# Kernel optimization log

Hardware: AMD Instinct MI355X
Metric: run time of the kernel (lower is better)

The kernel has to match this reference:

```python
import jax, jax.numpy as jnp
import numpy as np

N_USERS = 100000
N_TWEETS = 100000
N_NODES = N_USERS + N_TWEETS
N_EDGES = 600000
D = 128


def lrelu(x):
    return jax.nn.leaky_relu(x, negative_slope=0.01)


def linear(x, W, b):
    # torch nn.Linear convention: W is [out, in]
    return x @ W.T + b


def rgcn_conv(x, edge_index, edge_type, weight, root, bias):
    """PyG RGCNConv with num_relations=2, aggr='mean', root weight + bias."""
    src, dst = edge_index[0], edge_index[1]
    m = x[src]  # [E, D] gathered source features
    out = x @ root + bias
    for r in range(weight.shape[0]):
        mask = (edge_type == r).astype(x.dtype)  # [E]
        s = jax.ops.segment_sum(m * mask[:, None], dst, num_segments=N_NODES)
        cnt = jax.ops.segment_sum(mask, dst, num_segments=N_NODES)
        mean = s / jnp.maximum(cnt, 1.0)[:, None]  # nodes w/o rel-r in-edges -> 0
        out = out + mean @ weight[r]
    return out


def setup_inputs() -> dict:
    key = jax.random.key(0)
    ks = jax.random.split(key, 24)

    def lin(k, out_d, in_d):
        k1, k2 = jax.random.split(k)
        s = 1.0 / np.sqrt(in_d)
        return (jax.random.uniform(k1, (out_d, in_d), jnp.float32, -s, s),
                jax.random.uniform(k2, (out_d,), jnp.float32, -s, s))

    des = jax.random.normal(ks[0], (N_USERS, 100), jnp.float32)
    tweet = jax.random.normal(ks[1], (N_TWEETS, 100), jnp.float32)
    num_prop = jax.random.normal(ks[2], (N_USERS, 6), jnp.float32)
    cat_prop = jax.random.normal(ks[3], (N_USERS, 11), jnp.float32)
    edge_index = jax.random.randint(ks[4], (2, N_EDGES), 0, N_NODES, jnp.int32)
    edge_type = jax.random.randint(ks[5], (N_EDGES,), 0, 2, jnp.int32)

    W_des, b_des = lin(ks[6], D // 2, 100)       # des -> 64
    W_num, b_num = lin(ks[7], D // 4, 6)         # num_prop -> 32
    W_cat, b_cat = lin(ks[8], D // 4, 11)        # cat_prop -> 32
    W_tw, b_tw = lin(ks[9], D, 100)              # tweet -> 128
    W_in, b_in = lin(ks[10], D, D)
    rgcn_w = jax.random.normal(ks[11], (2, D, D), jnp.float32) / np.sqrt(D)
    rgcn_root = jax.random.normal(ks[12], (D, D), jnp.float32) / np.sqrt(D)
    rgcn_bias = jnp.zeros((D,), jnp.float32)
    W_o1, b_o1 = lin(ks[13], D, D)
    W_o2, b_o2 = lin(ks[14], 2, D)

    return dict(des=des, tweet=tweet, num_prop=num_prop, cat_prop=cat_prop,
                edge_index=edge_index, edge_type=edge_type,
                W_des=W_des, b_des=b_des, W_num=W_num, b_num=b_num,
                W_cat=W_cat, b_cat=b_cat, W_tw=W_tw, b_tw=b_tw,
                W_in=W_in, b_in=b_in, rgcn_w=rgcn_w, rgcn_root=rgcn_root,
                rgcn_bias=rgcn_bias, W_o1=W_o1, b_o1=b_o1, W_o2=W_o2, b_o2=b_o2)


def reference(des, tweet, num_prop, cat_prop, edge_index, edge_type,
              W_des, b_des, W_num, b_num, W_cat, b_cat, W_tw, b_tw,
              W_in, b_in, rgcn_w, rgcn_root, rgcn_bias, W_o1, b_o1, W_o2, b_o2):
    d = lrelu(linear(des, W_des, b_des))
    n = lrelu(linear(num_prop, W_num, b_num))
    c = lrelu(linear(cat_prop, W_cat, b_cat))
    x_users = jnp.concatenate([d, n, c], axis=1)       # [N_users, 128]
    t = lrelu(linear(tweet, W_tw, b_tw))               # [N_tweets, 128]
    x = jnp.concatenate([x_users, t], axis=0)          # [N_nodes, 128]
    x = lrelu(linear(x, W_in, b_in))
    x = rgcn_conv(x, edge_index, edge_type, rgcn_w, rgcn_root, rgcn_bias)
    # dropout in eval mode = identity
    x = rgcn_conv(x, edge_index, edge_type, rgcn_w, rgcn_root, rgcn_bias)
    x = lrelu(linear(x, W_o1, b_o1))
    return linear(x, W_o2, b_o2)
```

## Files before the change

### kernel.cpp

```cpp
#include <hip/hip_runtime.h>
#include <hip/hip_bf16.h>

typedef __hip_bfloat16 bf16;

typedef __bf16 bfv8 __attribute__((ext_vector_type(8)));
typedef float f32x4 __attribute__((ext_vector_type(4)));

__device__ __forceinline__ float lrelu(float x) { return x > 0.f ? x : 0.01f * x; }

__device__ __forceinline__ float ldv(float v) { return v; }
__device__ __forceinline__ float ldv(bf16 v) { return __bfloat162float(v); }
__device__ __forceinline__ void stv(float* p, float v) { *p = v; }
__device__ __forceinline__ void stv(bf16* p, float v) { *p = __float2bfloat16(v); }

__device__ __forceinline__ float in_rd(const void* p, size_t i, int isbf) {
  return isbf ? __bfloat162float(((const bf16*)p)[i]) : ((const float*)p)[i];
}
__device__ __forceinline__ int ix_rd(const void* p, size_t i, int is64) {
  return is64 ? (int)((const long long*)p)[i] : ((const int*)p)[i];
}

struct ProbeArgs {
  const void* p[23];
  int s[23];
  int mode[23];
};

__global__ void detect_all(ProbeArgs a, int* __restrict__ flags) {
  __shared__ int sh[256];
  int b = blockIdx.x;
  const unsigned int* w = (const unsigned int*)a.p[b];
  int s = a.s[b], mode = a.mode[b];
  int t = threadIdx.x;
  int c = 0;
  if (t < s) {
    if (mode == 0) {
      unsigned int v = w[t];
      int e = (v >> 7) & 0xFF;
      c = (e >= 100 && e <= 140) ? 1 : 0;
    } else {
      c = (w[2 * t + 1] == 0u) ? 1 : 0;
    }
  }
  sh[t] = c;
  __syncthreads();
  for (int d = 128; d; d >>= 1) {
    if (t < d) sh[t] += sh[t + d];
    __syncthreads();
  }
  if (t == 0) flags[b] = (mode == 0) ? (sh[0] * 10 >= 7 * s) : (sh[0] * 10 >= 9 * s);
}

#define PW_F32 82562
#define BF_BASE 82564
#define PW_W_TOTAL (BF_BASE + 5 * 8192)
#define ENC_BASE PW_W_TOTAL
#define ENC_N 33024
#define PW_TOTAL (ENC_BASE + 16384 + 256)
__global__ void setup_all(const void* Win, const void* bin, const void* rw, const void* root,
                          const void* rb, const void* Wo1, const void* bo1, const void* Wo2,
                          const void* bo2, const void* Wd, const void* bd, const void* Wn,
                          const void* bn, const void* Wc, const void* bc, const void* Wt,
                          const void* bt, const int* __restrict__ fl, int dDes, int dNum,
                          int dCat, int dTw, float* __restrict__ pw, int* __restrict__ cnt4,
                          int NNr) {
  int i = blockIdx.x * 256 + threadIdx.x;
  if (i < PW_W_TOTAL) {
    if (i < 16384) {
      int k = i >> 7, o = i & 127;
      pw[i] = in_rd(Win, (size_t)o * 128 + k, fl[14]);
    } else if (i < 32768) {
      int j = i - 16384;
      int k = j >> 7, o = j & 127;
      pw[i] = in_rd(Wo1, (size_t)o * 128 + k, fl[19]);
    } else if (i < 49152) {
      pw[i] = in_rd(root, i - 32768, fl[17]);
    } else if (i < 81920) {
      pw[i] = in_rd(rw, i - 49152, fl[16]);
    } else if (i < 82048) {
      pw[i] = in_rd(bin, i - 81920, fl[15]);
    } else if (i < 82176) {
      pw[i] = in_rd(rb, i - 82048, fl[18]);
    } else if (i < 82304) {
      pw[i] = in_rd(bo1, i - 82176, fl[20]);
    } else if (i < 82560) {
      pw[i] = in_rd(Wo2, i - 82304, fl[21]);
    } else if (i < PW_F32) {
      pw[i] = in_rd(bo2, i - 82560, fl[22]);
    } else if (i >= BF_BASE) {
      int j = i - BF_BASE;
      bf16* bw = (bf16*)(pw + BF_BASE);
#pragma unroll
      for (int q = 0; q < 2; q++) {
        int u = 2 * j + q;
        int m = u >> 14, r = u & 16383;
        int n = r >> 7, k = r & 127;
        float v;
        if (m == 0) v = in_rd(Win, (size_t)n * 128 + k, fl[14]);
        else if (m == 1) v = in_rd(Wo1, (size_t)n * 128 + k, fl[19]);
        else if (m == 2) v = in_rd(root, (size_t)k * 128 + n, fl[17]);
        else v = in_rd(rw, (size_t)(m - 3) * 16384 + (size_t)k * 128 + n, fl[16]);
        bw[u] = __float2bfloat16(v);
      }
    }
  } else if (i < PW_W_TOTAL + ENC_N) {
    int j = i - PW_W_TOTAL;
    bf16* e = (bf16*)(pw + ENC_BASE);
    float* bU = pw + ENC_BASE + 16384;
    float* bT = bU + 128;
    if (j < 16384) {
      int n = j >> 7, k = j & 127;
      float v = 0.f;
      if (n < 64) {
        if (k < dDes) v = in_rd(Wd, (size_t)n * dDes + k, fl[6]);
      } else if (n < 96) {
        int kk = k - dDes;
        if (kk >= 0 && kk < dNum) v = in_rd(Wn, (size_t)(n - 64) * dNum + kk, fl[8]);
      } else {
        int kk = k - dDes - dNum;
        if (kk >= 0 && kk < dCat) v = in_rd(Wc, (size_t)(n - 96) * dCat + kk, fl[10]);
      }
      e[j] = __float2bfloat16(v);
    } else if (j < 32768) {
      int j2 = j - 16384;
      int n = j2 >> 7, k = j2 & 127;
      float v = (k < dTw) ? in_rd(Wt, (size_t)n * dTw + k, fl[12]) : 0.f;
      e[j] = __float2bfloat16(v);
    } else if (j < 32896) {
      int j2 = j - 32768;
      bU[j2] = (j2 < 64) ? in_rd(bd, j2, fl[7])
                         : (j2 < 96) ? in_rd(bn, j2 - 64, fl[9]) : in_rd(bc, j2 - 96, fl[11]);
    } else {
      bT[j - 32896] = in_rd(bt, j - 32896, fl[13]);
    }
  } else {
    int j = i - PW_W_TOTAL - ENC_N;
    if (j < 4 * NNr) cnt4[j] = 0;
  }
}

__global__ void sig_fill(float* __restrict__ p, int n, float v) {
  int i = blockIdx.x * 256 + threadIdx.x;
  if (i < n) p[i] = v;
}

__global__ void count_edges(const void* __restrict__ ei, const void* __restrict__ et,
                            const int* __restrict__ fl, int* __restrict__ cnt, int NEr,
                            int NNr) {
  int e = blockIdx.x * 256 + threadIdx.x;
  if (e >= NEr) return;
  int d = ix_rd(ei, (size_t)NEr + e, fl[4]);
  int r = ix_rd(et, e, fl[5]) & 1;
  if ((unsigned)d >= (unsigned)NNr) return;
  atomicAdd(&cnt[r * NNr + d], 1);
}

__global__ void scan_blocks(const int* __restrict__ in, int* __restrict__ out,
                            int* __restrict__ bsum, int n) {
  __shared__ int sh[256];
  int t = threadIdx.x;
  int base = blockIdx.x * 1024 + t * 4;
  int a[4];
  int s = 0;
#pragma unroll
  for (int i = 0; i < 4; i++) {
    a[i] = (base + i < n) ? in[base + i] : 0;
    s += a[i];
  }
  sh[t] = s;
  __syncthreads();
  for (int d = 1; d < 256; d <<= 1) {
    int v = (t >= d) ? sh[t - d] : 0;
    __syncthreads();
    sh[t] += v;
    __syncthreads();
  }
  int ex = sh[t] - s;
#pragma unroll
  for (int i = 0; i < 4; i++) {
    if (base + i < n) out[base + i] = ex;
    ex += a[i];
  }
  if (t == 255 && bsum) bsum[blockIdx.x] = sh[255];
}

__global__ void scan_add_inv(int* __restrict__ off, const int* __restrict__ bsumsc,
                             const int* __restrict__ cnt, float* __restrict__ inv, int n) {
  int i = blockIdx.x * 256 + threadIdx.x;
  if (i >= n) return;
  off[i] += bsumsc[i >> 10];
  inv[i] = 1.f / fmaxf((float)cnt[i], 1.f);
}

__global__ void fill_elist(const void* __restrict__ ei, const void* __restrict__ et,
                           const int* __restrict__ fl, const int* __restrict__ off,
                           int* __restrict__ fill, int* __restrict__ elist, int NEr, int NNr) {
  int e = blockIdx.x * 256 + threadIdx.x;
  if (e >= NEr) return;
  int s = ix_rd(ei, e, fl[4]);
  int d = ix_rd(ei, (size_t)NEr + e, fl[4]);
  int r = ix_rd(et, e, fl[5]) & 1;
  if ((unsigned)d >= (unsigned)NNr || (unsigned)s >= (unsigned)NNr) return;
  int idx = r * NNr + d;
  int slot = off[idx] + atomicAdd(&fill[idx], 1);
  elist[slot] = s | ((d & 127) << 24);
}

__global__ __launch_bounds__(256) void enc_gemm(const void* __restrict__ A,
                                                const void* __restrict__ W,
                                                const void* __restrict__ B,
                                                const int* __restrict__ fl, int fa, int fw,
                                                int fb, bf16* __restrict__ x, int M, int K,
                                                int N, int row0, int col0) {
  __shared__ float Wb[128 * 102];
  __shared__ float bb[128];
  int t = threadIdx.x;
  int stride = (K & 1) ? K : K + 1;
  int fA = fl[fa];
  {
    int fW = fl[fw], fB = fl[fb];
    for (int idx = t; idx < N * K; idx += 256) {
      int j = idx / K, k = idx - j * K;
      Wb[j * stride + k] = in_rd(W, (size_t)j * K + k, fW);
    }
    if (t < N) bb[t] = in_rd(B, t, fB);
  }
  __syncthreads();
  int j = t % N;
  int r = t / N;
  int R = 256 / N;
  int iEnd = blockIdx.x * 64 + 64;
  if (iEnd > M) iEnd = M;
  const float* wrow = &Wb[j * stride];
  if (!fA) {
    const float* Af = (const float*)A;
    for (int i = blockIdx.x * 64 + r; i < iEnd; i += R) {
      const float* a = Af + (size_t)i * K;
      float acc = bb[j];
      for (int k = 0; k < K; k++) acc += a[k] * wrow[k];
      stv(&x[(size_t)(row0 + i) * 128 + col0 + j], lrelu(acc));
    }
  } else {
    const bf16* Ab = (const bf16*)A;
    for (int i = blockIdx.x * 64 + r; i < iEnd; i += R) {
      const bf16* a = Ab + (size_t)i * K;
      float acc = bb[j];
      for (int k = 0; k < K; k++) acc += __bfloat162float(a[k]) * wrow[k];
      stv(&x[(size_t)(row0 + i) * 128 + col0 + j], lrelu(acc));
    }
  }
}


__global__ __launch_bounds__(256) void enc_mfma(
    const void* __restrict__ A0, const void* __restrict__ A1, const void* __restrict__ A2,
    const int* __restrict__ fl, int fi0, int fi1, int fi2, int K0, int K1, int K2,
    const bf16* __restrict__ WbE, const float* __restrict__ biasE,
    const bf16* __restrict__ WbL, const float* __restrict__ bL, bf16* __restrict__ x,
    int M, int row0) {
  __shared__ __align__(16) bf16 Xs[16384];
  int t = threadIdx.x;
  int i0 = blockIdx.x * 128;

  {
    uint4 z = {0u, 0u, 0u, 0u};
#pragma unroll
    for (int i = 0; i < 8; i++) *(uint4*)((char*)Xs + i * 4096 + t * 16) = z;
  }
  __syncthreads();

  const void* As[3] = {A0, A1, A2};
  int Ks_[3] = {K0, K1, K2};
  int fis[3] = {fi0, fi1, fi2};
  int cb = 0;
  for (int s = 0; s < 3; s++) {
    int Ks = Ks_[s];
    if (Ks <= 0) continue;
    int isbf = fl[fis[s]];
    int total = 128 * Ks;
    long gml = (long)(M - i0) * Ks;
    int gmax = gml > total ? total : (gml < 0 ? 0 : (int)gml);
    int nu = (total + 3) >> 2;
    if (!isbf) {
      const float* Af = (const float*)As[s] + (size_t)i0 * Ks;
      for (int u = t; u < nu; u += 256) {
        int f0 = u * 4;
        float vv[4];
        if (f0 + 4 <= gmax) {
          float4 x4 = *(const float4*)(Af + f0);
          vv[0] = x4.x; vv[1] = x4.y; vv[2] = x4.z; vv[3] = x4.w;
        } else {
          vv[0] = (f0 < gmax) ? Af[f0] : 0.f;
          vv[1] = (f0 + 1 < gmax) ? Af[f0 + 1] : 0.f;
          vv[2] = (f0 + 2 < gmax) ? Af[f0 + 2] : 0.f;
          vv[3] = (f0 + 3 < gmax) ? Af[f0 + 3] : 0.f;
        }
#pragma unroll
        for (int q = 0; q < 4; q++) {
          int f = f0 + q;
          if (f < total) {
            int row = f / Ks, k = f - row * Ks;
            int byte = row * 256 + (cb + k) * 2;
            *(bf16*)((char*)Xs + (byte ^ ((row & 7) << 4))) = __float2bfloat16(vv[q]);
          }
        }
      }
    } else {
      const unsigned short* Ab = (const unsigned short*)As[s] + (size_t)i0 * Ks;
      for (int u = t; u < nu; u += 256) {
        int f0 = u * 4;
        unsigned short vv[4];
        if (f0 + 4 <= gmax) {
          ushort4 x4 = *(const ushort4*)(Ab + f0);
          vv[0] = x4.x; vv[1] = x4.y; vv[2] = x4.z; vv[3] = x4.w;
        } else {
          vv[0] = (f0 < gmax) ? Ab[f0] : 0;
          vv[1] = (f0 + 1 < gmax) ? Ab[f0 + 1] : 0;
          vv[2] = (f0 + 2 < gmax) ? Ab[f0 + 2] : 0;
          vv[3] = (f0 + 3 < gmax) ? Ab[f0 + 3] : 0;
        }
#pragma unroll
        for (int q = 0; q < 4; q++) {
          int f = f0 + q;
          if (f < total) {
            int row = f / Ks, k = f - row * Ks;
            int byte = row * 256 + (cb + k) * 2;
            *(unsigned short*)((char*)Xs + (byte ^ ((row & 7) << 4))) = vv[q];
          }
        }
      }
    }
    cb += Ks;
  }
  __syncthreads();

  int wv = t >> 6, l = t & 63;
  int lr = l & 15, lg = l >> 4;
  int rbase = (wv >> 1) * 64, cbase = (wv & 1) * 64;
  int ko = lg * 8;
  f32x4 acc[4][4] = {};
#pragma unroll
  for (int ks = 0; ks < 4; ks++) {
    bfv8 bk[4];
#pragma unroll
    for (int cg = 0; cg < 4; cg++)
      bk[cg] = *(const bfv8*)&WbE[(size_t)(cbase + cg * 16 + lr) * 128 + ks * 32 + ko];
    bfv8 af[4];
#pragma unroll
    for (int rg = 0; rg < 4; rg++) {
      int mrow = rbase + rg * 16 + lr;
      int byte = mrow * 256 + (ks * 32 + ko) * 2;
      af[rg] = *(const bfv8*)((const char*)Xs + (byte ^ ((mrow & 7) << 4)));
    }
#pragma unroll
    for (int rg = 0; rg < 4; rg++)
#pragma unroll
      for (int cg = 0; cg < 4; cg++)
        acc[rg][cg] =
            __builtin_amdgcn_mfma_f32_16x16x32_bf16(af[rg], bk[cg], acc[rg][cg], 0, 0, 0);
  }
  __syncthreads();

#pragma unroll
  for (int cg = 0; cg < 4; cg++) {
    int col = cbase + cg * 16 + lr;
    float bv = biasE[col];
#pragma unroll
    for (int rg = 0; rg < 4; rg++) {
      int r0 = rbase + rg * 16 + lg * 4;
#pragma unroll
      for (int j = 0; j < 4; j++) {
        int row = r0 + j;
        int byte = row * 256 + col * 2;
        *(bf16*)((char*)Xs + (byte ^ ((row & 7) << 4))) =
            __float2bfloat16(lrelu(acc[rg][cg][j] + bv));
      }
    }
  }
  __syncthreads();

  f32x4 acc2[4][4] = {};
#pragma unroll
  for (int ks = 0; ks < 4; ks++) {
    bfv8 bk[4];
#pragma unroll
    for (int cg = 0; cg < 4; cg++)
      bk[cg] = *(const bfv8*)&WbL[(size_t)(cbase + cg * 16 + lr) * 128 + ks * 32 + ko];
    bfv8 af[4];
#pragma unroll
    for (int rg = 0; rg < 4; rg++) {
      int mrow = rbase + rg * 16 + lr;
      int byte = mrow * 256 + (ks * 32 + ko) * 2;
      af[rg] = *(const bfv8*)((const char*)Xs + (byte ^ ((mrow & 7) << 4)));
    }
#pragma unroll
    for (int rg = 0; rg < 4; rg++)
#pragma unroll
      for (int cg = 0; cg < 4; cg++)
        acc2[rg][cg] =
            __builtin_amdgcn_mfma_f32_16x16x32_bf16(af[rg], bk[cg], acc2[rg][cg], 0, 0, 0);
  }

#pragma unroll
  for (int cg = 0; cg < 4; cg++) {
    int col = cbase + cg * 16 + lr;
    float bv = bL[col];
#pragma unroll
    for (int rg = 0; rg < 4; rg++) {
      int r0 = i0 + rbase + rg * 16 + lg * 4;
#pragma unroll
      for (int j = 0; j < 4; j++) {
        int row = r0 + j;
        if (row < M)
          x[(size_t)(row0 + row) * 128 + col] = __float2bfloat16(lrelu(acc2[rg][cg][j] + bv));
      }
    }
  }
}

__global__ __launch_bounds__(256) void mfma_lin(const bf16* __restrict__ A,
                                                const bf16* __restrict__ Wb,
                                                const float* __restrict__ bias,
                                                bf16* __restrict__ Out, int M) {
  int t = threadIdx.x;
  int wv = t >> 6, l = t & 63;
  int lr = l & 15, lg = l >> 4;
  int i0 = blockIdx.x * 128;
  int rbase = (wv >> 1) * 64;
  int cbase = (wv & 1) * 64;
  int ko = lg * 8;

  size_t rowoff[4];
#pragma unroll
  for (int rg = 0; rg < 4; rg++) {
    int row = i0 + rbase + rg * 16 + lr;
    if (row > M - 1) row = M - 1;
    rowoff[rg] = (size_t)row * 128;
  }

  bfv8 bfr[4][4];
#pragma unroll
  for (int cg = 0; cg < 4; cg++)
#pragma unroll
    for (int ks = 0; ks < 4; ks++)
      bfr[cg][ks] = *(const bfv8*)&Wb[(size_t)(cbase + cg * 16 + lr) * 128 + ks * 32 + ko];

  f32x4 acc[4][4] = {};
#pragma unroll
  for (int ks = 0; ks < 4; ks++) {
    bfv8 af[4];
#pragma unroll
    for (int rg = 0; rg < 4; rg++) af[rg] = *(const bfv8*)&A[rowoff[rg] + ks * 32 + ko];
#pragma unroll
    for (int rg = 0; rg < 4; rg++)
#pragma unroll
      for (int cg = 0; cg < 4; cg++)
        acc[rg][cg] =
            __builtin_amdgcn_mfma_f32_16x16x32_bf16(af[rg], bfr[cg][ks], acc[rg][cg], 0, 0, 0);
  }

#pragma unroll
  for (int cg = 0; cg < 4; cg++) {
    int col = cbase + cg * 16 + lr;
    float bv = bias[col];
#pragma unroll
    for (int rg = 0; rg < 4; rg++) {
      int row0 = i0 + rbase + rg * 16 + lg * 4;
#pragma unroll
      for (int j = 0; j < 4; j++) {
        int row = row0 + j;
        if (row < M) Out[(size_t)row * 128 + col] = __float2bfloat16(lrelu(acc[rg][cg][j] + bv));
      }
    }
  }
}

template <bool TAIL>
__global__ __launch_bounds__(256, 4) void mfma_conv_f(
    const bf16* __restrict__ X, const int* __restrict__ off, const int* __restrict__ cnt,
    const int* __restrict__ elist, const float* __restrict__ inv,
    const bf16* __restrict__ WB, const float* __restrict__ bias, bf16* __restrict__ Out,
    const bf16* __restrict__ Wo1B, const float* __restrict__ bO1,
    const float* __restrict__ Wo2, const float* __restrict__ bo2,
    float* __restrict__ out2, int M, int NNr) {
  __shared__ __align__(16) float At[64 * 128];
  int t = threadIdx.x;
  int wv = t >> 6, l = t & 63;
  int lr = l & 15, lg = l >> 4;
  int i0 = blockIdx.x * 32;
  int cbase = wv * 32;
  int ko = lg * 8;

  {
    int grp = t >> 4;
    int c8 = (t & 15) * 8;
    int stc[4], dgc[4];
#pragma unroll
    for (int pn = 0; pn < 4; pn++) {
      int vr = grp + pn * 16;
      int rel = vr >> 5, m = vr & 31;
      int node = i0 + m;
      bool ok = node < M;
      int idx = rel * NNr + node;
      stc[pn] = ok ? off[idx] : 0;
      dgc[pn] = ok ? cnt[idx] : 0;
    }
    int dmax = max(max(dgc[0], dgc[1]), max(dgc[2], dgc[3]));
    float s[4][8] = {};
    bfv8 v[4];
#pragma unroll
    for (int pn = 0; pn < 4; pn++) {
      if (dgc[pn] > 0) {
        int src = elist[stc[pn]] & 0xFFFFFF;
        v[pn] = *(const bfv8*)&X[(size_t)src * 128 + c8];
      }
    }
    for (int e = 0; e < dmax; e++) {
      bfv8 nv[4];
#pragma unroll
      for (int pn = 0; pn < 4; pn++) {
        if (e + 1 < dgc[pn]) {
          int src = elist[stc[pn] + e + 1] & 0xFFFFFF;
          nv[pn] = *(const bfv8*)&X[(size_t)src * 128 + c8];
        }
      }
#pragma unroll
      for (int pn = 0; pn < 4; pn++) {
        if (e < dgc[pn]) {
#pragma unroll
          for (int j = 0; j < 8; j++) s[pn][j] += __bfloat162float(v[pn][j]);
        }
      }
#pragma unroll
      for (int pn = 0; pn < 4; pn++) v[pn] = nv[pn];
    }
#pragma unroll
    for (int pn = 0; pn < 4; pn++) {
      int vr = grp + pn * 16;
      int sw = (vr & 7) << 4;
      int lb = vr * 512 + c8 * 4;
      *(float4*)((char*)At + (lb ^ sw)) = make_float4(s[pn][0], s[pn][1], s[pn][2], s[pn][3]);
      *(float4*)((char*)At + ((lb + 16) ^ sw)) =
          make_float4(s[pn][4], s[pn][5], s[pn][6], s[pn][7]);
    }
  }

  size_t rowoff[2];
  float iv0[2], iv1[2];
#pragma unroll
  for (int rg = 0; rg < 2; rg++) {
    int row = i0 + rg * 16 + lr;
    int rc = row < M ? row : M - 1;
    rowoff[rg] = (size_t)rc * 128;
    iv0[rg] = row < M ? inv[row] : 0.f;
    iv1[rg] = row < M ? inv[NNr + row] : 0.f;
  }

  f32x4 acc[2][2] = {};

#pragma unroll
  for (int ks = 0; ks < 4; ks++) {
    bfv8 bk[2];
#pragma unroll
    for (int cg = 0; cg < 2; cg++)
      bk[cg] = *(const bfv8*)&WB[(size_t)(cbase + cg * 16 + lr) * 128 + ks * 32 + ko];
    bfv8 af[2];
#pragma unroll
    for (int rg = 0; rg < 2; rg++) af[rg] = *(const bfv8*)&X[rowoff[rg] + ks * 32 + ko];
#pragma unroll
    for (int rg = 0; rg < 2; rg++)
#pragma unroll
      for (int cg = 0; cg < 2; cg++)
        acc[rg][cg] =
            __builtin_amdgcn_mfma_f32_16x16x32_bf16(af[rg], bk[cg], acc[rg][cg], 0, 0, 0);
  }
  __syncthreads();

#pragma unroll
  for (int r = 0; r < 2; r++) {
    const bf16* Wb = WB + 16384 * (1 + r);
#pragma unroll
    for (int ks = 0; ks < 4; ks++) {
      bfv8 bk[2];
#pragma unroll
      for (int cg = 0; cg < 2; cg++)
        bk[cg] = *(const bfv8*)&Wb[(size_t)(cbase + cg * 16 + lr) * 128 + ks * 32 + ko];
      bfv8 af[2];
#pragma unroll
      for (int rg = 0; rg < 2; rg++) {
        int mrow = r * 32 + rg * 16 + lr;
        int lb = mrow * 512 + ks * 128 + ko * 4;
        int sw = (mrow & 7) << 4;
        float4 f0 = *(const float4*)((const char*)At + (lb ^ sw));
        float4 f1 = *(const float4*)((const char*)At + ((lb + 16) ^ sw));
        float iv = r ? iv1[rg] : iv0[rg];
        bfv8 a;
        a[0] = (__bf16)(f0.x * iv); a[1] = (__bf16)(f0.y * iv);
        a[2] = (__bf16)(f0.z * iv); a[3] = (__bf16)(f0.w * iv);
        a[4] = (__bf16)(f1.x * iv); a[5] = (__bf16)(f1.y * iv);
        a[6] = (__bf16)(f1.z * iv); a[7] = (__bf16)(f1.w * iv);
        af[rg] = a;
      }
#pragma unroll
      for (int rg = 0; rg < 2; rg++)
#pragma unroll
        for (int cg = 0; cg < 2; cg++)
          acc[rg][cg] =
              __builtin_amdgcn_mfma_f32_16x16x32_bf16(af[rg], bk[cg], acc[rg][cg], 0, 0, 0);
    }
  }

  if (!TAIL) {
#pragma unroll
    for (int cg = 0; cg < 2; cg++) {
      int col = cbase + cg * 16 + lr;
      float bv = bias[col];
#pragma unroll
      for (int rg = 0; rg < 2; rg++) {
        int row0 = i0 + rg * 16 + lg * 4;
#pragma unroll
        for (int j = 0; j < 4; j++) {
          int row = row0 + j;
          if (row < M) Out[(size_t)row * 128 + col] = __float2bfloat16(acc[rg][cg][j] + bv);
        }
      }
    }
  } else {
    __syncthreads();
#pragma unroll
    for (int cg = 0; cg < 2; cg++) {
      int col = cbase + cg * 16 + lr;
      float bv = bias[col];
#pragma unroll
      for (int rg = 0; rg < 2; rg++) {
#pragma unroll
        for (int j = 0; j < 4; j++) {
          int row32 = rg * 16 + lg * 4 + j;
          int byte = row32 * 256 + col * 2;
          *(bf16*)((char*)At + (byte ^ ((row32 & 7) << 4))) =
              __float2bfloat16(acc[rg][cg][j] + bv);
        }
      }
    }
    __syncthreads();

    f32x4 acc2[2][2] = {};
#pragma unroll
    for (int ks = 0; ks < 4; ks++) {
      bfv8 bk[2];
#pragma unroll
      for (int cg = 0; cg < 2; cg++)
        bk[cg] = *(const bfv8*)&Wo1B[(size_t)(cbase + cg * 16 + lr) * 128 + ks * 32 + ko];
      bfv8 af[2];
#pragma unroll
      for (int rg = 0; rg < 2; rg++) {
        int mrow = rg * 16 + lr;
        int byte = mrow * 256 + (ks * 32 + ko) * 2;
        af[rg] = *(const bfv8*)((const char*)At + (byte ^ ((mrow & 7) << 4)));
      }
#pragma unroll
      for (int rg = 0; rg < 2; rg++)
#pragma unroll
        for (int cg = 0; cg < 2; cg++)
          acc2[rg][cg] =
              __builtin_amdgcn_mfma_f32_16x16x32_bf16(af[rg], bk[cg], acc2[rg][cg], 0, 0, 0);
    }
#pragma unroll
    for (int cg = 0; cg < 2; cg++) {
      int col = cbase + cg * 16 + lr;
      float bv = bO1[col];
#pragma unroll
      for (int rg = 0; rg < 2; rg++) {
#pragma unroll
        for (int j = 0; j < 4; j++) {
          int row32 = rg * 16 + lg * 4 + j;
          *(bf16*)((char*)At + 8192 + row32 * 256 + col * 2) =
              __float2bfloat16(lrelu(acc2[rg][cg][j] + bv));
        }
      }
    }
    __syncthreads();

    int row = t >> 3, seg = t & 7;
    const bf16* zr = (const bf16*)((const char*)At + 8192 + row * 256 + seg * 32);
    float p0 = 0.f, p1 = 0.f;
#pragma unroll
    for (int q = 0; q < 16; q++) {
      float xv = __bfloat162float(zr[q]);
      int col = seg * 16 + q;
      p0 += xv * Wo2[col];
      p1 += xv * Wo2[128 + col];
    }
#pragma unroll
    for (int o = 4; o; o >>= 1) {
      p0 += __shfl_down(p0, o, 8);
      p1 += __shfl_down(p1, o, 8);
    }
    int grow = i0 + row;
    if (seg == 0 && grow < M) {
      out2[(size_t)grow * 2] = p0 + bo2[0];
      out2[(size_t)grow * 2 + 1] = p1 + bo2[1];
    }
  }
}

static void run_pipeline(void* const* d_in, const int* S, float* out, char* ws,
                         int NUr, int NTr, int NEr, int dDes, int dNum, int dCat, int dTw,
                         hipStream_t stream) {
  const int NNr = NUr + NTr;
  const size_t xbytes = (size_t)NNr * 128 * 2;

  bf16* xa = (bf16*)ws;
  bf16* xb = (bf16*)(ws + xbytes);
  char* p = ws + 2 * xbytes;
  int* cnt = (int*)p;      p += (size_t)2 * NNr * 4;
  int* fill = (int*)p;     p += (size_t)2 * NNr * 4;
  int* off = (int*)p;      p += (size_t)2 * NNr * 4;
  int* bsum = (int*)p;     p += 2048 * 4;
  int* bsumsc = (int*)p;   p += 2048 * 4;
  float* inv = (float*)p;  p += (size_t)2 * NNr * 4;
  int* elist = (int*)p;    p += (size_t)NEr * 4;
  float* pw = (float*)p;   p += (size_t)PW_TOTAL * 4;
  int* flags = (int*)p;

  ProbeArgs pa;
  for (int i = 0; i < 23; i++) {
    int src = (i == 22) ? 21 : i;
    pa.p[i] = d_in[src];
    if (i == 4) {
      pa.mode[i] = 1;
      pa.s[i] = NEr < 256 ? NEr : 256;
    } else if (i == 5) {
      pa.mode[i] = 1;
      int s2 = NEr / 2 < 256 ? NEr / 2 : 256;
      pa.s[i] = s2 < 1 ? 1 : s2;
    } else {
      pa.mode[i] = 0;
      int s = S[src] / 2;
      if (s > 256) s = 256;
      if (s < 1) s = 1;
      pa.s[i] = s;
    }
  }
  detect_all<<<23, 256, 0, stream>>>(pa, flags);

  const int setupN = PW_W_TOTAL + ENC_N + 4 * NNr;
  setup_all<<<(setupN + 255) / 256, 256, 0, stream>>>(
      d_in[14], d_in[15], d_in[16], d_in[17], d_in[18], d_in[19], d_in[20], d_in[21],
      d_in[22], d_in[6], d_in[7], d_in[8], d_in[9], d_in[10], d_in[11], d_in[12], d_in[13],
      flags, dDes, dNum, dCat, dTw, pw, cnt, NNr);

  const float* bIn = pw + 81920;
  const float* rbp = pw + 82048;
  const float* bO1 = pw + 82176;
  const float* Wo2p = pw + 82304;
  const float* bo2p = pw + 82560;
  const bf16* WinB = (const bf16*)(pw + BF_BASE);
  const bf16* Wo1B = (const bf16*)(pw + BF_BASE + 8192);
  const bf16* ConvB = (const bf16*)(pw + BF_BASE + 16384);
  const bf16* EncU = (const bf16*)(pw + ENC_BASE);
  const bf16* EncT = (const bf16*)(pw + ENC_BASE + 8192);
  const float* bU = pw + ENC_BASE + 16384;
  const float* bT = bU + 128;

  const void* ei = d_in[4];
  const void* et = d_in[5];
  const int nb1 = (2 * NNr + 1023) / 1024;

  count_edges<<<(NEr + 255) / 256, 256, 0, stream>>>(ei, et, flags, cnt, NEr, NNr);
  scan_blocks<<<nb1, 256, 0, stream>>>(cnt, off, bsum, 2 * NNr);
  scan_blocks<<<1, 256, 0, stream>>>(bsum, bsumsc, nullptr, nb1);
  scan_add_inv<<<(2 * NNr + 255) / 256, 256, 0, stream>>>(off, bsumsc, cnt, inv, 2 * NNr);
  fill_elist<<<(NEr + 255) / 256, 256, 0, stream>>>(ei, et, flags, off, fill, elist, NEr, NNr);

  if (dDes + dNum + dCat <= 128 && dTw <= 128) {
    enc_mfma<<<(NUr + 127) / 128, 256, 0, stream>>>(d_in[0], d_in[2], d_in[3], flags, 0, 2, 3,
                                                    dDes, dNum, dCat, EncU, bU, WinB, bIn, xb,
                                                    NUr, 0);
    enc_mfma<<<(NTr + 127) / 128, 256, 0, stream>>>(d_in[1], nullptr, nullptr, flags, 1, 1, 1,
                                                    dTw, 0, 0, EncT, bT, WinB, bIn, xb, NTr,
                                                    NUr);
  } else {
    enc_gemm<<<(NUr + 63) / 64, 256, 0, stream>>>(d_in[0], d_in[6], d_in[7], flags, 0, 6, 7,
                                                  xa, NUr, dDes, 64, 0, 0);
    enc_gemm<<<(NUr + 63) / 64, 256, 0, stream>>>(d_in[2], d_in[8], d_in[9], flags, 2, 8, 9,
                                                  xa, NUr, dNum, 32, 0, 64);
    enc_gemm<<<(NUr + 63) / 64, 256, 0, stream>>>(d_in[3], d_in[10], d_in[11], flags, 3, 10,
                                                  11, xa, NUr, dCat, 32, 0, 96);
    enc_gemm<<<(NTr + 63) / 64, 256, 0, stream>>>(d_in[1], d_in[12], d_in[13], flags, 1, 12,
                                                  13, xa, NTr, dTw, 128, NUr, 0);
    mfma_lin<<<(NNr + 127) / 128, 256, 0, stream>>>(xa, WinB, bIn, xb, NNr);
  }

  const int mt32 = (NNr + 31) / 32;
  mfma_conv_f<false><<<mt32, 256, 0, stream>>>(xb, off, cnt, elist, inv, ConvB, rbp, xa,
                                               nullptr, nullptr, nullptr, nullptr, nullptr,
                                               NNr, NNr);
  mfma_conv_f<true><<<mt32, 256, 0, stream>>>(xa, off, cnt, elist, inv, ConvB, rbp, nullptr,
                                              Wo1B, bO1, Wo2p, bo2p, out, NNr, NNr);
}

extern "C" void kernel_launch(void* const* d_in, const int* in_sizes, int n_in,
                              void* d_out, int out_size, void* d_ws, size_t ws_size,
                              hipStream_t stream) {
  float* out = (float*)d_out;
  char* ws = (char*)d_ws;

  auto signal = [&](int k) {
    sig_fill<<<(out_size + 255) / 256, 256, 0, stream>>>(out, out_size, (float)(200 + k));
  };

  if (n_in != 23) { signal(1); return; }
  const int* S = in_sizes;
  if (S[7] != 64 || S[9] != 32 || S[11] != 32 || S[13] != 128) { signal(2); return; }
  if (S[15] != 128) { signal(3); return; }
  if (S[6] % 64 || S[8] % 32 || S[10] % 32 || S[12] % 128) { signal(4); return; }
  int dDes = S[6] / 64, dNum = S[8] / 32, dCat = S[10] / 32, dTw = S[12] / 128;
  if (dDes <= 0 || dTw <= 0 || S[0] % dDes || S[1] % dTw) { signal(5); return; }
  if (dDes > 101 || dNum > 101 || dCat > 101 || dTw > 101) { signal(4); return; }
  int NUr = S[0] / dDes, NTr = S[1] / dTw, NNr = NUr + NTr, NEr = S[5];
  if (S[2] != NUr * dNum || S[3] != NUr * dCat) { signal(5); return; }
  if (S[4] != 2 * NEr || NEr < 1024) { signal(6); return; }
  if (NNr >= (1 << 24)) { signal(6); return; }
  if (S[14] != 16384 || S[16] != 32768 || S[17] != 16384 || S[18] != 128 ||
      S[19] != 16384 || S[20] != 128 || S[21] != 256 || S[22] != 2) { signal(7); return; }
  if (out_size != NNr * 2) { signal(8); return; }

  const size_t smallBytes = (size_t)4 * ((size_t)2 * NNr * 4) + 2 * 2048 * 4 +
                            (size_t)NEr * 4 + (size_t)PW_TOTAL * 4 + 512;
  const size_t need = 2 * (size_t)NNr * 128 * 2 + smallBytes;

  if (ws_size >= need) {
    run_pipeline(d_in, S, out, ws, NUr, NTr, NEr, dDes, dNum, dCat, dTw, stream);
  } else {
    signal(9);
  }
}
```

Measured before the change: 491.1 us.

## Merge preprocessing kernels to cut launches and drop the inverse-count buffer

Zeroing of the count buffers moves into extra blocks of the detect kernel, and edge counting moves into the setup kernel. The scan-add/inverse kernel is removed: consumers add the block-sum offset inline and compute 1/max(cnt,1) on the fly. The two encoder launches are merged into one grid that picks the user or tweet path per block. This cuts kernel launches and one full pass over the offset arrays, at the cost of a little extra per-thread arithmetic in the conv kernels.

```diff
diff --git a/kernel.cpp b/kernel.cpp
--- a/kernel.cpp
+++ b/kernel.cpp
@@ -26,12 +26,18 @@
   int mode[23];
 };
 
-__global__ void detect_all(ProbeArgs a, int* __restrict__ flags) {
+__global__ void detect_all(ProbeArgs a, int* __restrict__ flags, int* __restrict__ cnt4,
+                           int nz) {
+  int b = blockIdx.x;
+  int t = threadIdx.x;
+  if (b >= 23) {
+    int j = (b - 23) * 256 + t;
+    if (j < nz) cnt4[j] = 0;
+    return;
+  }
   __shared__ int sh[256];
-  int b = blockIdx.x;
   const unsigned int* w = (const unsigned int*)a.p[b];
   int s = a.s[b], mode = a.mode[b];
-  int t = threadIdx.x;
   int c = 0;
   if (t < s) {
     if (mode == 0) {
@@ -61,9 +67,9 @@
                           const void* rb, const void* Wo1, const void* bo1, const void* Wo2,
                           const void* bo2, const void* Wd, const void* bd, const void* Wn,
                           const void* bn, const void* Wc, const void* bc, const void* Wt,
-                          const void* bt, const int* __restrict__ fl, int dDes, int dNum,
-                          int dCat, int dTw, float* __restrict__ pw, int* __restrict__ cnt4,
-                          int NNr) {
+                          const void* bt, const void* ei, const void* et,
+                          const int* __restrict__ fl, int dDes, int dNum, int dCat, int dTw,
+                          float* __restrict__ pw, int* __restrict__ cnt, int NNr, int NEr) {
   int i = blockIdx.x * 256 + threadIdx.x;
   if (i < PW_W_TOTAL) {
     if (i < 16384) {
@@ -134,25 +140,18 @@
       bT[j - 32896] = in_rd(bt, j - 32896, fl[13]);
     }
   } else {
-    int j = i - PW_W_TOTAL - ENC_N;
-    if (j < 4 * NNr) cnt4[j] = 0;
+    int e = i - PW_W_TOTAL - ENC_N;
+    if (e < NEr) {
+      int d = ix_rd(ei, (size_t)NEr + e, fl[4]);
+      int r = ix_rd(et, e, fl[5]) & 1;
+      if ((unsigned)d < (unsigned)NNr) atomicAdd(&cnt[r * NNr + d], 1);
+    }
   }
 }
 
 __global__ void sig_fill(float* __restrict__ p, int n, float v) {
   int i = blockIdx.x * 256 + threadIdx.x;
   if (i < n) p[i] = v;
-}
-
-__global__ void count_edges(const void* __restrict__ ei, const void* __restrict__ et,
-                            const int* __restrict__ fl, int* __restrict__ cnt, int NEr,
-                            int NNr) {
-  int e = blockIdx.x * 256 + threadIdx.x;
-  if (e >= NEr) return;
-  int d = ix_rd(ei, (size_t)NEr + e, fl[4]);
-  int r = ix_rd(et, e, fl[5]) & 1;
-  if ((unsigned)d >= (unsigned)NNr) return;
-  atomicAdd(&cnt[r * NNr + d], 1);
 }
 
 __global__ void scan_blocks(const int* __restrict__ in, int* __restrict__ out,
@@ -184,17 +183,10 @@
   if (t == 255 && bsum) bsum[blockIdx.x] = sh[255];
 }
 
-__global__ void scan_add_inv(int* __restrict__ off, const int* __restrict__ bsumsc,
-                             const int* __restrict__ cnt, float* __restrict__ inv, int n) {
-  int i = blockIdx.x * 256 + threadIdx.x;
-  if (i >= n) return;
-  off[i] += bsumsc[i >> 10];
-  inv[i] = 1.f / fmaxf((float)cnt[i], 1.f);
-}
-
 __global__ void fill_elist(const void* __restrict__ ei, const void* __restrict__ et,
                            const int* __restrict__ fl, const int* __restrict__ off,
-                           int* __restrict__ fill, int* __restrict__ elist, int NEr, int NNr) {
+                           const int* __restrict__ bsumsc, int* __restrict__ fill,
+                           int* __restrict__ elist, int NEr, int NNr) {
   int e = blockIdx.x * 256 + threadIdx.x;
   if (e >= NEr) return;
   int s = ix_rd(ei, e, fl[4]);
@@ -202,7 +194,7 @@
   int r = ix_rd(et, e, fl[5]) & 1;
   if ((unsigned)d >= (unsigned)NNr || (unsigned)s >= (unsigned)NNr) return;
   int idx = r * NNr + d;
-  int slot = off[idx] + atomicAdd(&fill[idx], 1);
+  int slot = off[idx] + bsumsc[idx >> 10] + atomicAdd(&fill[idx], 1);
   elist[slot] = s | ((d & 127) << 24);
 }
 
@@ -253,14 +245,32 @@
 
 
 __global__ __launch_bounds__(256) void enc_mfma(
-    const void* __restrict__ A0, const void* __restrict__ A1, const void* __restrict__ A2,
-    const int* __restrict__ fl, int fi0, int fi1, int fi2, int K0, int K1, int K2,
-    const bf16* __restrict__ WbE, const float* __restrict__ biasE,
+    const void* __restrict__ Ad, const void* __restrict__ An, const void* __restrict__ Ac,
+    const void* __restrict__ Atw, const int* __restrict__ fl, int dDes, int dNum, int dCat,
+    int dTw, const bf16* __restrict__ EncU, const float* __restrict__ bU,
+    const bf16* __restrict__ EncT, const float* __restrict__ bT,
     const bf16* __restrict__ WbL, const float* __restrict__ bL, bf16* __restrict__ x,
-    int M, int row0) {
+    int NUr, int NTr, int ublocks) {
   __shared__ __align__(16) bf16 Xs[16384];
   int t = threadIdx.x;
-  int i0 = blockIdx.x * 128;
+  int b = blockIdx.x;
+
+  const void* As[3];
+  int Ks_[3], fis[3];
+  const bf16* WbE;
+  const float* biasE;
+  int M, row0, i0;
+  if (b < ublocks) {
+    As[0] = Ad; As[1] = An; As[2] = Ac;
+    Ks_[0] = dDes; Ks_[1] = dNum; Ks_[2] = dCat;
+    fis[0] = 0; fis[1] = 2; fis[2] = 3;
+    WbE = EncU; biasE = bU; M = NUr; row0 = 0; i0 = b * 128;
+  } else {
+    As[0] = Atw; As[1] = nullptr; As[2] = nullptr;
+    Ks_[0] = dTw; Ks_[1] = 0; Ks_[2] = 0;
+    fis[0] = 1; fis[1] = 1; fis[2] = 1;
+    WbE = EncT; biasE = bT; M = NTr; row0 = NUr; i0 = (b - ublocks) * 128;
+  }
 
   {
     uint4 z = {0u, 0u, 0u, 0u};
@@ -269,9 +279,6 @@
   }
   __syncthreads();
 
-  const void* As[3] = {A0, A1, A2};
-  int Ks_[3] = {K0, K1, K2};
-  int fis[3] = {fi0, fi1, fi2};
   int cb = 0;
   for (int s = 0; s < 3; s++) {
     int Ks = Ks_[s];
@@ -478,7 +485,7 @@
 template <bool TAIL>
 __global__ __launch_bounds__(256, 4) void mfma_conv_f(
     const bf16* __restrict__ X, const int* __restrict__ off, const int* __restrict__ cnt,
-    const int* __restrict__ elist, const float* __restrict__ inv,
+    const int* __restrict__ bsumsc, const int* __restrict__ elist,
     const bf16* __restrict__ WB, const float* __restrict__ bias, bf16* __restrict__ Out,
     const bf16* __restrict__ Wo1B, const float* __restrict__ bO1,
     const float* __restrict__ Wo2, const float* __restrict__ bo2,
@@ -502,7 +509,7 @@
       int node = i0 + m;
       bool ok = node < M;
       int idx = rel * NNr + node;
-      stc[pn] = ok ? off[idx] : 0;
+      stc[pn] = ok ? off[idx] + bsumsc[idx >> 10] : 0;
       dgc[pn] = ok ? cnt[idx] : 0;
     }
     int dmax = max(max(dgc[0], dgc[1]), max(dgc[2], dgc[3]));
@@ -552,8 +559,8 @@
     int row = i0 + rg * 16 + lr;
     int rc = row < M ? row : M - 1;
     rowoff[rg] = (size_t)rc * 128;
-    iv0[rg] = row < M ? inv[row] : 0.f;
-    iv1[rg] = row < M ? inv[NNr + row] : 0.f;
+    iv0[rg] = row < M ? 1.f / fmaxf((float)cnt[row], 1.f) : 0.f;
+    iv1[rg] = row < M ? 1.f / fmaxf((float)cnt[NNr + row], 1.f) : 0.f;
   }
 
   f32x4 acc[2][2] = {};
@@ -718,7 +725,6 @@
   int* off = (int*)p;      p += (size_t)2 * NNr * 4;
   int* bsum = (int*)p;     p += 2048 * 4;
   int* bsumsc = (int*)p;   p += 2048 * 4;
-  float* inv = (float*)p;  p += (size_t)2 * NNr * 4;
   int* elist = (int*)p;    p += (size_t)NEr * 4;
   float* pw = (float*)p;   p += (size_t)PW_TOTAL * 4;
   int* flags = (int*)p;
@@ -742,13 +748,14 @@
       pa.s[i] = s;
     }
   }
-  detect_all<<<23, 256, 0, stream>>>(pa, flags);
-
-  const int setupN = PW_W_TOTAL + ENC_N + 4 * NNr;
+  const int nz = 4 * NNr;
+  detect_all<<<23 + (nz + 255) / 256, 256, 0, stream>>>(pa, flags, cnt, nz);
+
+  const int setupN = PW_W_TOTAL + ENC_N + NEr;
   setup_all<<<(setupN + 255) / 256, 256, 0, stream>>>(
       d_in[14], d_in[15], d_in[16], d_in[17], d_in[18], d_in[19], d_in[20], d_in[21],
       d_in[22], d_in[6], d_in[7], d_in[8], d_in[9], d_in[10], d_in[11], d_in[12], d_in[13],
-      flags, dDes, dNum, dCat, dTw, pw, cnt, NNr);
+      d_in[4], d_in[5], flags, dDes, dNum, dCat, dTw, pw, cnt, NNr, NEr);
 
   const float* bIn = pw + 81920;
   const float* rbp = pw + 82048;
@@ -767,19 +774,17 @@
   const void* et = d_in[5];
   const int nb1 = (2 * NNr + 1023) / 1024;
 
-  count_edges<<<(NEr + 255) / 256, 256, 0, stream>>>(ei, et, flags, cnt, NEr, NNr);
   scan_blocks<<<nb1, 256, 0, stream>>>(cnt, off, bsum, 2 * NNr);
   scan_blocks<<<1, 256, 0, stream>>>(bsum, bsumsc, nullptr, nb1);
-  scan_add_inv<<<(2 * NNr + 255) / 256, 256, 0, stream>>>(off, bsumsc, cnt, inv, 2 * NNr);
-  fill_elist<<<(NEr + 255) / 256, 256, 0, stream>>>(ei, et, flags, off, fill, elist, NEr, NNr);
+  fill_elist<<<(NEr + 255) / 256, 256, 0, stream>>>(ei, et, flags, off, bsumsc, fill, elist,
+                                                    NEr, NNr);
 
   if (dDes + dNum + dCat <= 128 && dTw <= 128) {
-    enc_mfma<<<(NUr + 127) / 128, 256, 0, stream>>>(d_in[0], d_in[2], d_in[3], flags, 0, 2, 3,
-                                                    dDes, dNum, dCat, EncU, bU, WinB, bIn, xb,
-                                                    NUr, 0);
-    enc_mfma<<<(NTr + 127) / 128, 256, 0, stream>>>(d_in[1], nullptr, nullptr, flags, 1, 1, 1,
-                                                    dTw, 0, 0, EncT, bT, WinB, bIn, xb, NTr,
-                                                    NUr);
+    const int ub = (NUr + 127) / 128;
+    const int tb = (NTr + 127) / 128;
+    enc_mfma<<<ub + tb, 256, 0, stream>>>(d_in[0], d_in[2], d_in[3], d_in[1], flags, dDes,
+                                          dNum, dCat, dTw, EncU, bU, EncT, bT, WinB, bIn, xb,
+                                          NUr, NTr, ub);
   } else {
     enc_gemm<<<(NUr + 63) / 64, 256, 0, stream>>>(d_in[0], d_in[6], d_in[7], flags, 0, 6, 7,
                                                   xa, NUr, dDes, 64, 0, 0);
@@ -793,11 +798,11 @@
   }
 
   const int mt32 = (NNr + 31) / 32;
-  mfma_conv_f<false><<<mt32, 256, 0, stream>>>(xb, off, cnt, elist, inv, ConvB, rbp, xa,
+  mfma_conv_f<false><<<mt32, 256, 0, stream>>>(xb, off, cnt, bsumsc, elist, ConvB, rbp, xa,
                                                nullptr, nullptr, nullptr, nullptr, nullptr,
                                                NNr, NNr);
-  mfma_conv_f<true><<<mt32, 256, 0, stream>>>(xa, off, cnt, elist, inv, ConvB, rbp, nullptr,
-                                              Wo1B, bO1, Wo2p, bo2p, out, NNr, NNr);
+  mfma_conv_f<true><<<mt32, 256, 0, stream>>>(xa, off, cnt, bsumsc, elist, ConvB, rbp,
+                                              nullptr, Wo1B, bO1, Wo2p, bo2p, out, NNr, NNr);
 }
 
 extern "C" void kernel_launch(void* const* d_in, const int* in_sizes, int n_in,
@@ -826,7 +831,7 @@
       S[19] != 16384 || S[20] != 128 || S[21] != 256 || S[22] != 2) { signal(7); return; }
   if (out_size != NNr * 2) { signal(8); return; }
 
-  const size_t smallBytes = (size_t)4 * ((size_t)2 * NNr * 4) + 2 * 2048 * 4 +
+  const size_t smallBytes = (size_t)3 * ((size_t)2 * NNr * 4) + 2 * 2048 * 4 +
                             (size_t)NEr * 4 + (size_t)PW_TOTAL * 4 + 512;
   const size_t need = 2 * (size_t)NNr * 128 * 2 + smallBytes;
 
```

Measured after the change: 495.6 us. Within noise of the previous version (+0.9%).
